# Kernel tuning notes

Measured on AMD Instinct MI355X. Metric: run time of the kernel, lower is better.

The kernel has to match this reference:

```python
import jax, jax.numpy as jnp
import numpy as np

H, D, BETA = 12, 64, 1.0
EPS = 1e-8


def setup_inputs() -> dict:
    key = jax.random.key(0)
    k1, k2 = jax.random.split(key)
    n, dim = 1024, H * D
    x = jax.random.normal(k1, (n, dim), dtype=jnp.float32)
    mask = jnp.ones((n, n), dtype=bool)
    W_qk = jax.random.normal(k2, (2 * H * D, dim), dtype=jnp.float32) / np.sqrt(dim).astype(np.float32)
    return {"x": x, "mask": mask, "W_qk": W_qk}


def _free_energy_heads(xh, mask, W_qk):
    # xh: (H, n, D) unit-norm token vectors per head -> per-head free energy (H,)
    n = xh.shape[1]
    xf = jnp.transpose(xh, (1, 0, 2)).reshape(n, H * D)      # 'h n d -> n (h d)'
    qk = xf @ W_qk.T                                          # (n, 2*H*D), Linear no-bias
    q, k = jnp.split(qk, 2, axis=-1)
    q = jnp.transpose(q.reshape(n, H, D), (1, 0, 2))          # (H, n, D)
    k = jnp.transpose(k.reshape(n, H, D), (1, 0, 2))
    sim = jnp.einsum('hid,hjd->hij', q, k)                    # (H, n, n)
    sim = jnp.where(mask, sim, jnp.finfo(sim.dtype).min)
    J = jax.scipy.special.logsumexp(sim, axis=-1)             # (H, n)
    # t* = root of quadratic: beta*t^2 + (-0.5 - 2 beta J) t + (beta J^2 + 0.5 J - 0.25 beta |x|^2)
    hn = jnp.sum(xh * xh, axis=-1)                            # (H, n), |x_i|^2
    b = -0.5 - 2.0 * BETA * J
    c = BETA * J ** 2 + 0.5 * J - 0.25 * BETA * hn
    t = (-b + jnp.sqrt(b * b - 4.0 * BETA * c)) / (2.0 * BETA)
    v = t - J                                                 # (H, n)
    inv_v = 1.0 / jnp.clip(v, EPS, jnp.finfo(v.dtype).max)    # safe_reciprocal
    phi = (BETA * jnp.sum(t, axis=-1)
           - 0.5 * jnp.sum(jnp.log(v + EPS), axis=-1)
           + 0.25 * BETA * jnp.sum(hn * inv_v, axis=-1))      # (H,)
    log_Z = -0.5 * n * (1.0 + jnp.log(2.0 * BETA)) + phi
    return -log_Z / BETA                                      # (H,)


def reference(x, mask, W_qk):
    n = x.shape[0]
    xh = jnp.transpose(x.reshape(n, H, D), (1, 0, 2))         # (H, n, D)
    xh = xh / jnp.linalg.norm(xh, axis=-1, keepdims=True)
    jac = jax.jacrev(lambda xs: _free_energy_heads(xs, mask, W_qk))(xh)  # (H, H, n, D)
    diag = jnp.diagonal(jac)                                  # (n, D, H): dF_h/dx_h only
    out = jnp.transpose(diag, (0, 2, 1)).reshape(n, H * D)    # 'n d h -> n (h d)'
    return -out
```

## Files before the change

kernel.cpp:

```cpp
#include <hip/hip_runtime.h>
#include <cstdint>

#define NTOK 1024
#define NH   12
#define HD   64
#define DIM  768
#define QKD  1536

static constexpr float C2G = 0.61803398874989485f;

typedef __bf16 bf16x8 __attribute__((ext_vector_type(8)));
typedef __bf16 bf16x4 __attribute__((ext_vector_type(4)));
typedef float  f32x4  __attribute__((ext_vector_type(4)));

#define MFMA16(a, b, c) __builtin_amdgcn_mfma_f32_16x16x32_bf16((a), (b), (c), 0, 0, 0)

#define FRAG(S, outer, ks) (*(const bf16x8*)&S[(outer) + (l & 15)][(ks) * 32 + (l >> 4) * 8])

__global__ __launch_bounds__(256) void prep_k(const float* __restrict__ x,
                                              const float* __restrict__ W,
                                              float* __restrict__ xf,
                                              __bf16* __restrict__ xhb,
                                              __bf16* __restrict__ Wb,
                                              __bf16* __restrict__ WT) {
  __shared__ float Ws[64][65];
  int b = blockIdx.x, t = threadIdx.x;
  if (b < 3072) {
    int gid  = b * 4 + (t >> 6);
    int lane = t & 63;
    int i = gid / NH, h = gid - i * NH;
    size_t idx = (size_t)i * DIM + h * HD + lane;
    float v = x[idx];
    float ss = v * v;
#pragma unroll
    for (int m = 1; m < 64; m <<= 1) ss += __shfl_xor(ss, m);
    float r = v * rsqrtf(ss);
    xf[idx] = r;
    xhb[idx] = (__bf16)r;
  } else if (b < 3072 + 1152) {
    int tg = (b - 3072) * 256 + t;
    float4 v = ((const float4*)W)[tg];
    bf16x4 o;
    o[0] = (__bf16)v.x; o[1] = (__bf16)v.y; o[2] = (__bf16)v.z; o[3] = (__bf16)v.w;
    *(bf16x4*)(Wb + (size_t)tg * 4) = o;
  } else {
    int bb = b - 3072 - 1152;
    int h = bb % NH, p = bb / NH;
    int rowbase = p * DIM + h * HD;
#pragma unroll
    for (int rr = 0; rr < 16; ++rr) {
      int row = rr * 4 + (t >> 6), col = t & 63;
      Ws[row][col] = W[(size_t)(rowbase + row) * DIM + h * HD + col];
    }
    __syncthreads();
    __bf16* dst = WT + ((size_t)p * NH + h) * HD * HD;
#pragma unroll
    for (int rr = 0; rr < 16; ++rr) {
      int dlt = rr * 4 + (t >> 6), d = t & 63;
      dst[dlt * HD + d] = (__bf16)Ws[d][dlt];
    }
  }
}

__global__ __launch_bounds__(256) void gemm_dual_k(const __bf16* __restrict__ A,
                                                   const __bf16* __restrict__ Bt,
                                                   __bf16* __restrict__ qkb,
                                                   __bf16* __restrict__ qkT) {
  __shared__ __align__(16) __bf16 As[64][72];
  __shared__ __align__(16) __bf16 Bs[64][72];
  int m0 = blockIdx.x * 64, n0 = blockIdx.y * 64;
  int t = threadIdx.x, l = t & 63, w = t >> 6;
  int R = (w >> 1) * 32, Cc = (w & 1) * 32;
  int srow = t >> 2, scol = (t & 3) * 16;
  f32x4 acc[2][2] = {};
  for (int k0 = 0; k0 < DIM; k0 += 64) {
    *(uint4*)&As[srow][scol]     = *(const uint4*)(A  + (size_t)(m0 + srow) * DIM + k0 + scol);
    *(uint4*)&As[srow][scol + 8] = *(const uint4*)(A  + (size_t)(m0 + srow) * DIM + k0 + scol + 8);
    *(uint4*)&Bs[srow][scol]     = *(const uint4*)(Bt + (size_t)(n0 + srow) * DIM + k0 + scol);
    *(uint4*)&Bs[srow][scol + 8] = *(const uint4*)(Bt + (size_t)(n0 + srow) * DIM + k0 + scol + 8);
    __syncthreads();
#pragma unroll
    for (int ks = 0; ks < 2; ++ks) {
      bf16x8 af[2], bf[2];
#pragma unroll
      for (int mf = 0; mf < 2; ++mf) af[mf] = FRAG(As, R + mf * 16, ks);
#pragma unroll
      for (int nf = 0; nf < 2; ++nf) bf[nf] = FRAG(Bs, Cc + nf * 16, ks);
#pragma unroll
      for (int mf = 0; mf < 2; ++mf)
#pragma unroll
        for (int nf = 0; nf < 2; ++nf) acc[mf][nf] = MFMA16(af[mf], bf[nf], acc[mf][nf]);
    }
    __syncthreads();
  }
#pragma unroll
  for (int mf = 0; mf < 2; ++mf)
#pragma unroll
    for (int nf = 0; nf < 2; ++nf) {
      int rowb = m0 + R + mf * 16 + (l >> 4) * 4;
      int col  = n0 + Cc + nf * 16 + (l & 15);
      bf16x4 o4;
#pragma unroll
      for (int r = 0; r < 4; ++r) {
        __bf16 v = (__bf16)acc[mf][nf][r];
        o4[r] = v;
        qkb[(size_t)(rowb + r) * QKD + col] = v;
      }
      *(bf16x4*)(qkT + (size_t)col * NTOK + rowb) = o4;
    }
}

__global__ __launch_bounds__(256) void kbar_k(const __bf16* __restrict__ qkb,
                                              const __bf16* __restrict__ qkT,
                                              __bf16* __restrict__ kbar,
                                              float* __restrict__ invZ) {
  __shared__ __align__(16) __bf16 Qs[64][72], Ks[2][64][72], KTs[2][64][72], Es[64][72];
  __shared__ float Zs[64];
  int i0 = blockIdx.x * 64, h = blockIdx.y;
  int t = threadIdx.x, l = t & 63, w = t >> 6;
  int R = (w >> 1) * 32, Cc = (w & 1) * 32;
  int srow = t >> 2, scol = (t & 3) * 16;
  const __bf16* kbase  = qkb + DIM + h * HD;
  const __bf16* ktbase = qkT + (size_t)(DIM + h * HD + srow) * NTOK;
  *(uint4*)&Qs[srow][scol]     = *(const uint4*)(qkb + (size_t)(i0 + srow) * QKD + h * HD + scol);
  *(uint4*)&Qs[srow][scol + 8] = *(const uint4*)(qkb + (size_t)(i0 + srow) * QKD + h * HD + scol + 8);
  if (t < 64) Zs[t] = 0.f;
  uint4 kA = *(const uint4*)(kbase + (size_t)srow * QKD + scol);
  uint4 kB = *(const uint4*)(kbase + (size_t)srow * QKD + scol + 8);
  uint4 tA = *(const uint4*)(ktbase + scol);
  uint4 tB = *(const uint4*)(ktbase + scol + 8);
  f32x4 facc[2][2] = {};
  float zacc[8] = {0.f, 0.f, 0.f, 0.f, 0.f, 0.f, 0.f, 0.f};
  for (int jt = 0; jt < 16; ++jt) {
    int buf = jt & 1;
    *(uint4*)&Ks[buf][srow][scol]      = kA;
    *(uint4*)&Ks[buf][srow][scol + 8]  = kB;
    *(uint4*)&KTs[buf][srow][scol]     = tA;
    *(uint4*)&KTs[buf][srow][scol + 8] = tB;
    if (jt < 15) {
      int j0 = (jt + 1) * 64;
      kA = *(const uint4*)(kbase + (size_t)(j0 + srow) * QKD + scol);
      kB = *(const uint4*)(kbase + (size_t)(j0 + srow) * QKD + scol + 8);
      tA = *(const uint4*)(ktbase + j0 + scol);
      tB = *(const uint4*)(ktbase + j0 + scol + 8);
    }
    __syncthreads();
    f32x4 sacc[2][2] = {};
#pragma unroll
    for (int ks = 0; ks < 2; ++ks) {
      bf16x8 af[2], bf[2];
#pragma unroll
      for (int mf = 0; mf < 2; ++mf) af[mf] = FRAG(Qs, R + mf * 16, ks);
#pragma unroll
      for (int nf = 0; nf < 2; ++nf) bf[nf] = FRAG(Ks[buf], Cc + nf * 16, ks);
#pragma unroll
      for (int mf = 0; mf < 2; ++mf)
#pragma unroll
        for (int nf = 0; nf < 2; ++nf) sacc[mf][nf] = MFMA16(af[mf], bf[nf], sacc[mf][nf]);
    }
#pragma unroll
    for (int mf = 0; mf < 2; ++mf)
#pragma unroll
      for (int r = 0; r < 4; ++r) {
        float e0 = __expf(sacc[mf][0][r]);
        float e1 = __expf(sacc[mf][1][r]);
        zacc[mf * 4 + r] += e0 + e1;
        int row = R + mf * 16 + (l >> 4) * 4 + r;
        Es[row][Cc + (l & 15)]      = (__bf16)e0;
        Es[row][Cc + 16 + (l & 15)] = (__bf16)e1;
      }
    __syncthreads();
#pragma unroll
    for (int ks = 0; ks < 2; ++ks) {
      bf16x8 af[2], bf[2];
#pragma unroll
      for (int mf = 0; mf < 2; ++mf) af[mf] = FRAG(Es, R + mf * 16, ks);
#pragma unroll
      for (int nf = 0; nf < 2; ++nf) bf[nf] = FRAG(KTs[buf], Cc + nf * 16, ks);
#pragma unroll
      for (int mf = 0; mf < 2; ++mf)
#pragma unroll
        for (int nf = 0; nf < 2; ++nf) facc[mf][nf] = MFMA16(af[mf], bf[nf], facc[mf][nf]);
    }
  }
#pragma unroll
  for (int zi = 0; zi < 8; ++zi) {
    float z = zacc[zi];
    z += __shfl_xor(z, 1); z += __shfl_xor(z, 2);
    z += __shfl_xor(z, 4); z += __shfl_xor(z, 8);
    if ((l & 15) == 0) {
      int row = R + (zi >> 2) * 16 + (l >> 4) * 4 + (zi & 3);
      atomicAdd(&Zs[row], z);
    }
  }
  __syncthreads();
  if (t < 64) {
    float iz = 1.0f / Zs[t];
    Zs[t] = iz;
    invZ[(size_t)h * NTOK + i0 + t] = iz;
  }
  __syncthreads();
#pragma unroll
  for (int mf = 0; mf < 2; ++mf)
#pragma unroll
    for (int nf = 0; nf < 2; ++nf)
#pragma unroll
      for (int r = 0; r < 4; ++r) {
        int row = R + mf * 16 + (l >> 4) * 4 + r;
        int col = Cc + nf * 16 + (l & 15);
        kbar[(size_t)(i0 + row) * DIM + h * HD + col] = (__bf16)(facc[mf][nf][r] * Zs[row]);
      }
}

__global__ __launch_bounds__(256) void qbar_final_k(const __bf16* __restrict__ qkb,
                                                    const __bf16* __restrict__ qkT,
                                                    const float* __restrict__ invZ,
                                                    const __bf16* __restrict__ kbar,
                                                    const __bf16* __restrict__ WT,
                                                    const float* __restrict__ xf,
                                                    float* __restrict__ out) {
  __shared__ __align__(16) __bf16 Ks[64][72], Qs[2][64][72], QTs[2][64][72], Es[64][72];
  int j0 = blockIdx.x * 64, h = blockIdx.y;
  int t = threadIdx.x, l = t & 63, w = t >> 6;
  int R = (w >> 1) * 32, Cc = (w & 1) * 32;
  int srow = t >> 2, scol = (t & 3) * 16;
  const __bf16* qbase  = qkb + h * HD;
  const __bf16* qtbase = qkT + (size_t)(h * HD + srow) * NTOK;
  const float*  izb    = invZ + (size_t)h * NTOK;
  *(uint4*)&Ks[srow][scol]     = *(const uint4*)(qkb + (size_t)(j0 + srow) * QKD + DIM + h * HD + scol);
  *(uint4*)&Ks[srow][scol + 8] = *(const uint4*)(qkb + (size_t)(j0 + srow) * QKD + DIM + h * HD + scol + 8);
  uint4 qA = *(const uint4*)(qbase + (size_t)srow * QKD + scol);
  uint4 qB = *(const uint4*)(qbase + (size_t)srow * QKD + scol + 8);
  uint4 tA = *(const uint4*)(qtbase + scol);
  uint4 tB = *(const uint4*)(qtbase + scol + 8);
  f32x4 facc[2][2] = {};
  for (int it = 0; it < 16; ++it) {
    int buf = it & 1;
    *(uint4*)&Qs[buf][srow][scol]      = qA;
    *(uint4*)&Qs[buf][srow][scol + 8]  = qB;
    *(uint4*)&QTs[buf][srow][scol]     = tA;
    *(uint4*)&QTs[buf][srow][scol + 8] = tB;
    if (it < 15) {
      int i0 = (it + 1) * 64;
      qA = *(const uint4*)(qbase + (size_t)(i0 + srow) * QKD + scol);
      qB = *(const uint4*)(qbase + (size_t)(i0 + srow) * QKD + scol + 8);
      tA = *(const uint4*)(qtbase + i0 + scol);
      tB = *(const uint4*)(qtbase + i0 + scol + 8);
    }
    __syncthreads();
    f32x4 sacc[2][2] = {};
#pragma unroll
    for (int ks = 0; ks < 2; ++ks) {
      bf16x8 af[2], bf[2];
#pragma unroll
      for (int mf = 0; mf < 2; ++mf) af[mf] = FRAG(Ks, R + mf * 16, ks);
#pragma unroll
      for (int nf = 0; nf < 2; ++nf) bf[nf] = FRAG(Qs[buf], Cc + nf * 16, ks);
#pragma unroll
      for (int mf = 0; mf < 2; ++mf)
#pragma unroll
        for (int nf = 0; nf < 2; ++nf) sacc[mf][nf] = MFMA16(af[mf], bf[nf], sacc[mf][nf]);
    }
    float iz0 = izb[it * 64 + Cc + (l & 15)];
    float iz1 = izb[it * 64 + Cc + 16 + (l & 15)];
#pragma unroll
    for (int mf = 0; mf < 2; ++mf)
#pragma unroll
      for (int r = 0; r < 4; ++r) {
        float e0 = __expf(sacc[mf][0][r]) * iz0;
        float e1 = __expf(sacc[mf][1][r]) * iz1;
        int row = R + mf * 16 + (l >> 4) * 4 + r;
        Es[row][Cc + (l & 15)]      = (__bf16)e0;
        Es[row][Cc + 16 + (l & 15)] = (__bf16)e1;
      }
    __syncthreads();
#pragma unroll
    for (int ks = 0; ks < 2; ++ks) {
      bf16x8 af[2], bf[2];
#pragma unroll
      for (int mf = 0; mf < 2; ++mf) af[mf] = FRAG(Es, R + mf * 16, ks);
#pragma unroll
      for (int nf = 0; nf < 2; ++nf) bf[nf] = FRAG(QTs[buf], Cc + nf * 16, ks);
#pragma unroll
      for (int mf = 0; mf < 2; ++mf)
#pragma unroll
        for (int nf = 0; nf < 2; ++nf) facc[mf][nf] = MFMA16(af[mf], bf[nf], facc[mf][nf]);
    }
  }
  __syncthreads();
#pragma unroll
  for (int mf = 0; mf < 2; ++mf)
#pragma unroll
    for (int nf = 0; nf < 2; ++nf)
#pragma unroll
      for (int r = 0; r < 4; ++r)
        Es[R + mf * 16 + (l >> 4) * 4 + r][Cc + nf * 16 + (l & 15)] = (__bf16)facc[mf][nf][r];
  const __bf16* wq = WT + (size_t)h * HD * HD;
  const __bf16* wk = WT + ((size_t)NH + h) * HD * HD;
  *(uint4*)&Ks[srow][scol]         = *(const uint4*)(kbar + (size_t)(j0 + srow) * DIM + h * HD + scol);
  *(uint4*)&Ks[srow][scol + 8]     = *(const uint4*)(kbar + (size_t)(j0 + srow) * DIM + h * HD + scol + 8);
  *(uint4*)&QTs[0][srow][scol]     = *(const uint4*)(wq + (size_t)srow * HD + scol);
  *(uint4*)&QTs[0][srow][scol + 8] = *(const uint4*)(wq + (size_t)srow * HD + scol + 8);
  *(uint4*)&Qs[0][srow][scol]      = *(const uint4*)(wk + (size_t)srow * HD + scol);
  *(uint4*)&Qs[0][srow][scol + 8]  = *(const uint4*)(wk + (size_t)srow * HD + scol + 8);
  __syncthreads();
  f32x4 acc2[2][2] = {};
#pragma unroll
  for (int ks = 0; ks < 2; ++ks) {
    bf16x8 af[2], bf[2];
#pragma unroll
    for (int mf = 0; mf < 2; ++mf) af[mf] = FRAG(Ks, R + mf * 16, ks);
#pragma unroll
    for (int nf = 0; nf < 2; ++nf) bf[nf] = FRAG(QTs[0], Cc + nf * 16, ks);
#pragma unroll
    for (int mf = 0; mf < 2; ++mf)
#pragma unroll
      for (int nf = 0; nf < 2; ++nf) acc2[mf][nf] = MFMA16(af[mf], bf[nf], acc2[mf][nf]);
  }
#pragma unroll
  for (int ks = 0; ks < 2; ++ks) {
    bf16x8 af[2], bf[2];
#pragma unroll
    for (int mf = 0; mf < 2; ++mf) af[mf] = FRAG(Es, R + mf * 16, ks);
#pragma unroll
    for (int nf = 0; nf < 2; ++nf) bf[nf] = FRAG(Qs[0], Cc + nf * 16, ks);
#pragma unroll
    for (int mf = 0; mf < 2; ++mf)
#pragma unroll
      for (int nf = 0; nf < 2; ++nf) acc2[mf][nf] = MFMA16(af[mf], bf[nf], acc2[mf][nf]);
  }
#pragma unroll
  for (int mf = 0; mf < 2; ++mf)
#pragma unroll
    for (int nf = 0; nf < 2; ++nf)
#pragma unroll
      for (int r = 0; r < 4; ++r) {
        int row = j0 + R + mf * 16 + (l >> 4) * 4 + r;
        int col = h * HD + Cc + nf * 16 + (l & 15);
        size_t idx = (size_t)row * DIM + col;
        out[idx] = acc2[mf][nf][r] + C2G * xf[idx];
      }
}

extern "C" void kernel_launch(void* const* d_in, const int* in_sizes, int n_in,
                              void* d_out, int out_size, void* d_ws, size_t ws_size,
                              hipStream_t stream) {
  const float* x = (const float*)d_in[0];
  const float* W = (const float*)d_in[2];
  float* out = (float*)d_out;

  float* wsf = (float*)d_ws;
  size_t off = 0;
  float* xf   = wsf + off; off += (size_t)NTOK * DIM;
  float* invZ = wsf + off; off += (size_t)NH * NTOK;
  __bf16* wsb = (__bf16*)(wsf + off);
  size_t boff = 0;
  __bf16* xhb  = wsb + boff; boff += (size_t)NTOK * DIM;
  __bf16* Wb   = wsb + boff; boff += (size_t)QKD * DIM;
  __bf16* WT   = wsb + boff; boff += (size_t)2 * NH * HD * HD;
  __bf16* qkb  = wsb + boff; boff += (size_t)NTOK * QKD;
  __bf16* qkT  = wsb + boff; boff += (size_t)QKD * NTOK;
  __bf16* kbar = wsb + boff; boff += (size_t)NTOK * DIM;

  prep_k<<<dim3(3072 + 1152 + 24), dim3(256), 0, stream>>>(x, W, xf, xhb, Wb, WT);
  gemm_dual_k<<<dim3(16, 24), dim3(256), 0, stream>>>(xhb, Wb, qkb, qkT);
  kbar_k<<<dim3(16, NH), dim3(256), 0, stream>>>(qkb, qkT, kbar, invZ);
  qbar_final_k<<<dim3(16, NH), dim3(256), 0, stream>>>(qkb, qkT, invZ, kbar, WT, xf, out);
}
```

Measured before the change: 55.92 us.

## Split attention reductions across two blocks and add a separate final combine kernel

The kbar and qbar kernels now split the 1024-long reduction into two halves, which doubles the grid from 192 to 384 blocks. Each block writes fp32 partial accumulators, and the row sums Z are accumulated with global atomics into a buffer that prep_k zeroes. A new final kernel adds the partials, normalises, and applies the W projections. The QK GEMM also gains a double-buffered LDS pipeline with register prefetch, which removes one barrier per k-step. The aim is to fill more of the GPU's compute units, at the cost of an extra launch, extra partial-buffer traffic and atomics.

New measurement: 50.53 us. 1.11x faster.

```diff
diff --git a/kernel.cpp b/kernel.cpp
--- a/kernel.cpp
+++ b/kernel.cpp
@@ -22,7 +22,8 @@
                                               float* __restrict__ xf,
                                               __bf16* __restrict__ xhb,
                                               __bf16* __restrict__ Wb,
-                                              __bf16* __restrict__ WT) {
+                                              __bf16* __restrict__ WT,
+                                              float* __restrict__ Zg) {
   __shared__ float Ws[64][65];
   int b = blockIdx.x, t = threadIdx.x;
   if (b < 3072) {
@@ -37,14 +38,14 @@
     float r = v * rsqrtf(ss);
     xf[idx] = r;
     xhb[idx] = (__bf16)r;
-  } else if (b < 3072 + 1152) {
+  } else if (b < 4224) {
     int tg = (b - 3072) * 256 + t;
     float4 v = ((const float4*)W)[tg];
     bf16x4 o;
     o[0] = (__bf16)v.x; o[1] = (__bf16)v.y; o[2] = (__bf16)v.z; o[3] = (__bf16)v.w;
     *(bf16x4*)(Wb + (size_t)tg * 4) = o;
-  } else {
-    int bb = b - 3072 - 1152;
+  } else if (b < 4248) {
+    int bb = b - 4224;
     int h = bb % NH, p = bb / NH;
     int rowbase = p * DIM + h * HD;
 #pragma unroll
@@ -59,6 +60,10 @@
       int dlt = rr * 4 + (t >> 6), d = t & 63;
       dst[dlt * HD + d] = (__bf16)Ws[d][dlt];
     }
+  } else {
+    int zz = b - 4248;
+    float4 z4 = make_float4(0.f, 0.f, 0.f, 0.f);
+    ((float4*)Zg)[zz * 256 + t] = z4;
   }
 }
 
@@ -66,32 +71,42 @@
                                                    const __bf16* __restrict__ Bt,
                                                    __bf16* __restrict__ qkb,
                                                    __bf16* __restrict__ qkT) {
-  __shared__ __align__(16) __bf16 As[64][72];
-  __shared__ __align__(16) __bf16 Bs[64][72];
+  __shared__ __align__(16) __bf16 As[2][64][72], Bs[2][64][72];
   int m0 = blockIdx.x * 64, n0 = blockIdx.y * 64;
   int t = threadIdx.x, l = t & 63, w = t >> 6;
   int R = (w >> 1) * 32, Cc = (w & 1) * 32;
   int srow = t >> 2, scol = (t & 3) * 16;
+  uint4 aA = *(const uint4*)(A  + (size_t)(m0 + srow) * DIM + scol);
+  uint4 aB = *(const uint4*)(A  + (size_t)(m0 + srow) * DIM + scol + 8);
+  uint4 bA = *(const uint4*)(Bt + (size_t)(n0 + srow) * DIM + scol);
+  uint4 bB = *(const uint4*)(Bt + (size_t)(n0 + srow) * DIM + scol + 8);
   f32x4 acc[2][2] = {};
-  for (int k0 = 0; k0 < DIM; k0 += 64) {
-    *(uint4*)&As[srow][scol]     = *(const uint4*)(A  + (size_t)(m0 + srow) * DIM + k0 + scol);
-    *(uint4*)&As[srow][scol + 8] = *(const uint4*)(A  + (size_t)(m0 + srow) * DIM + k0 + scol + 8);
-    *(uint4*)&Bs[srow][scol]     = *(const uint4*)(Bt + (size_t)(n0 + srow) * DIM + k0 + scol);
-    *(uint4*)&Bs[srow][scol + 8] = *(const uint4*)(Bt + (size_t)(n0 + srow) * DIM + k0 + scol + 8);
+  for (int kt = 0; kt < 12; ++kt) {
+    int buf = kt & 1;
+    *(uint4*)&As[buf][srow][scol]     = aA;
+    *(uint4*)&As[buf][srow][scol + 8] = aB;
+    *(uint4*)&Bs[buf][srow][scol]     = bA;
+    *(uint4*)&Bs[buf][srow][scol + 8] = bB;
+    if (kt < 11) {
+      int k0 = (kt + 1) * 64;
+      aA = *(const uint4*)(A  + (size_t)(m0 + srow) * DIM + k0 + scol);
+      aB = *(const uint4*)(A  + (size_t)(m0 + srow) * DIM + k0 + scol + 8);
+      bA = *(const uint4*)(Bt + (size_t)(n0 + srow) * DIM + k0 + scol);
+      bB = *(const uint4*)(Bt + (size_t)(n0 + srow) * DIM + k0 + scol + 8);
+    }
     __syncthreads();
 #pragma unroll
     for (int ks = 0; ks < 2; ++ks) {
       bf16x8 af[2], bf[2];
 #pragma unroll
-      for (int mf = 0; mf < 2; ++mf) af[mf] = FRAG(As, R + mf * 16, ks);
-#pragma unroll
-      for (int nf = 0; nf < 2; ++nf) bf[nf] = FRAG(Bs, Cc + nf * 16, ks);
+      for (int mf = 0; mf < 2; ++mf) af[mf] = FRAG(As[buf], R + mf * 16, ks);
+#pragma unroll
+      for (int nf = 0; nf < 2; ++nf) bf[nf] = FRAG(Bs[buf], Cc + nf * 16, ks);
 #pragma unroll
       for (int mf = 0; mf < 2; ++mf)
 #pragma unroll
         for (int nf = 0; nf < 2; ++nf) acc[mf][nf] = MFMA16(af[mf], bf[nf], acc[mf][nf]);
     }
-    __syncthreads();
   }
 #pragma unroll
   for (int mf = 0; mf < 2; ++mf)
@@ -110,13 +125,15 @@
     }
 }
 
-__global__ __launch_bounds__(256) void kbar_k(const __bf16* __restrict__ qkb,
-                                              const __bf16* __restrict__ qkT,
-                                              __bf16* __restrict__ kbar,
-                                              float* __restrict__ invZ) {
+__global__ __launch_bounds__(256) void kbarp_k(const __bf16* __restrict__ qkb,
+                                               const __bf16* __restrict__ qkT,
+                                               float* __restrict__ part_k,
+                                               float* __restrict__ Zg) {
   __shared__ __align__(16) __bf16 Qs[64][72], Ks[2][64][72], KTs[2][64][72], Es[64][72];
-  __shared__ float Zs[64];
-  int i0 = blockIdx.x * 64, h = blockIdx.y;
+  int u = blockIdx.x;
+  int h = u >> 5, rem = u & 31;
+  int i0 = (rem >> 1) * 64;
+  int jt0 = (rem & 1) * 8;
   int t = threadIdx.x, l = t & 63, w = t >> 6;
   int R = (w >> 1) * 32, Cc = (w & 1) * 32;
   int srow = t >> 2, scol = (t & 3) * 16;
@@ -124,20 +141,19 @@
   const __bf16* ktbase = qkT + (size_t)(DIM + h * HD + srow) * NTOK;
   *(uint4*)&Qs[srow][scol]     = *(const uint4*)(qkb + (size_t)(i0 + srow) * QKD + h * HD + scol);
   *(uint4*)&Qs[srow][scol + 8] = *(const uint4*)(qkb + (size_t)(i0 + srow) * QKD + h * HD + scol + 8);
-  if (t < 64) Zs[t] = 0.f;
-  uint4 kA = *(const uint4*)(kbase + (size_t)srow * QKD + scol);
-  uint4 kB = *(const uint4*)(kbase + (size_t)srow * QKD + scol + 8);
-  uint4 tA = *(const uint4*)(ktbase + scol);
-  uint4 tB = *(const uint4*)(ktbase + scol + 8);
+  uint4 kA = *(const uint4*)(kbase + (size_t)(jt0 * 64 + srow) * QKD + scol);
+  uint4 kB = *(const uint4*)(kbase + (size_t)(jt0 * 64 + srow) * QKD + scol + 8);
+  uint4 tA = *(const uint4*)(ktbase + jt0 * 64 + scol);
+  uint4 tB = *(const uint4*)(ktbase + jt0 * 64 + scol + 8);
   f32x4 facc[2][2] = {};
   float zacc[8] = {0.f, 0.f, 0.f, 0.f, 0.f, 0.f, 0.f, 0.f};
-  for (int jt = 0; jt < 16; ++jt) {
+  for (int jt = jt0; jt < jt0 + 8; ++jt) {
     int buf = jt & 1;
     *(uint4*)&Ks[buf][srow][scol]      = kA;
     *(uint4*)&Ks[buf][srow][scol + 8]  = kB;
     *(uint4*)&KTs[buf][srow][scol]     = tA;
     *(uint4*)&KTs[buf][srow][scol + 8] = tB;
-    if (jt < 15) {
+    if (jt < jt0 + 7) {
       int j0 = (jt + 1) * 64;
       kA = *(const uint4*)(kbase + (size_t)(j0 + srow) * QKD + scol);
       kB = *(const uint4*)(kbase + (size_t)(j0 + srow) * QKD + scol + 8);
@@ -183,6 +199,17 @@
         for (int nf = 0; nf < 2; ++nf) facc[mf][nf] = MFMA16(af[mf], bf[nf], facc[mf][nf]);
     }
   }
+  float* pk = part_k + (size_t)u * 4096;
+#pragma unroll
+  for (int mf = 0; mf < 2; ++mf)
+#pragma unroll
+    for (int nf = 0; nf < 2; ++nf)
+#pragma unroll
+      for (int r = 0; r < 4; ++r) {
+        int row = R + mf * 16 + (l >> 4) * 4 + r;
+        int col = Cc + nf * 16 + (l & 15);
+        pk[row * 64 + col] = facc[mf][nf][r];
+      }
 #pragma unroll
   for (int zi = 0; zi < 8; ++zi) {
     float z = zacc[zi];
@@ -190,57 +217,40 @@
     z += __shfl_xor(z, 4); z += __shfl_xor(z, 8);
     if ((l & 15) == 0) {
       int row = R + (zi >> 2) * 16 + (l >> 4) * 4 + (zi & 3);
-      atomicAdd(&Zs[row], z);
-    }
-  }
-  __syncthreads();
-  if (t < 64) {
-    float iz = 1.0f / Zs[t];
-    Zs[t] = iz;
-    invZ[(size_t)h * NTOK + i0 + t] = iz;
-  }
-  __syncthreads();
-#pragma unroll
-  for (int mf = 0; mf < 2; ++mf)
-#pragma unroll
-    for (int nf = 0; nf < 2; ++nf)
-#pragma unroll
-      for (int r = 0; r < 4; ++r) {
-        int row = R + mf * 16 + (l >> 4) * 4 + r;
-        int col = Cc + nf * 16 + (l & 15);
-        kbar[(size_t)(i0 + row) * DIM + h * HD + col] = (__bf16)(facc[mf][nf][r] * Zs[row]);
-      }
-}
-
-__global__ __launch_bounds__(256) void qbar_final_k(const __bf16* __restrict__ qkb,
-                                                    const __bf16* __restrict__ qkT,
-                                                    const float* __restrict__ invZ,
-                                                    const __bf16* __restrict__ kbar,
-                                                    const __bf16* __restrict__ WT,
-                                                    const float* __restrict__ xf,
-                                                    float* __restrict__ out) {
+      atomicAdd(&Zg[(size_t)h * NTOK + i0 + row], z);
+    }
+  }
+}
+
+__global__ __launch_bounds__(256) void qbarp_k(const __bf16* __restrict__ qkb,
+                                               const __bf16* __restrict__ qkT,
+                                               const float* __restrict__ Zg,
+                                               float* __restrict__ part_q) {
   __shared__ __align__(16) __bf16 Ks[64][72], Qs[2][64][72], QTs[2][64][72], Es[64][72];
-  int j0 = blockIdx.x * 64, h = blockIdx.y;
+  int u = blockIdx.x;
+  int h = u >> 5, rem = u & 31;
+  int j0 = (rem >> 1) * 64;
+  int it0 = (rem & 1) * 8;
   int t = threadIdx.x, l = t & 63, w = t >> 6;
   int R = (w >> 1) * 32, Cc = (w & 1) * 32;
   int srow = t >> 2, scol = (t & 3) * 16;
   const __bf16* qbase  = qkb + h * HD;
   const __bf16* qtbase = qkT + (size_t)(h * HD + srow) * NTOK;
-  const float*  izb    = invZ + (size_t)h * NTOK;
+  const float*  zb     = Zg + (size_t)h * NTOK;
   *(uint4*)&Ks[srow][scol]     = *(const uint4*)(qkb + (size_t)(j0 + srow) * QKD + DIM + h * HD + scol);
   *(uint4*)&Ks[srow][scol + 8] = *(const uint4*)(qkb + (size_t)(j0 + srow) * QKD + DIM + h * HD + scol + 8);
-  uint4 qA = *(const uint4*)(qbase + (size_t)srow * QKD + scol);
-  uint4 qB = *(const uint4*)(qbase + (size_t)srow * QKD + scol + 8);
-  uint4 tA = *(const uint4*)(qtbase + scol);
-  uint4 tB = *(const uint4*)(qtbase + scol + 8);
+  uint4 qA = *(const uint4*)(qbase + (size_t)(it0 * 64 + srow) * QKD + scol);
+  uint4 qB = *(const uint4*)(qbase + (size_t)(it0 * 64 + srow) * QKD + scol + 8);
+  uint4 tA = *(const uint4*)(qtbase + it0 * 64 + scol);
+  uint4 tB = *(const uint4*)(qtbase + it0 * 64 + scol + 8);
   f32x4 facc[2][2] = {};
-  for (int it = 0; it < 16; ++it) {
+  for (int it = it0; it < it0 + 8; ++it) {
     int buf = it & 1;
     *(uint4*)&Qs[buf][srow][scol]      = qA;
     *(uint4*)&Qs[buf][srow][scol + 8]  = qB;
     *(uint4*)&QTs[buf][srow][scol]     = tA;
     *(uint4*)&QTs[buf][srow][scol + 8] = tB;
-    if (it < 15) {
+    if (it < it0 + 7) {
       int i0 = (it + 1) * 64;
       qA = *(const uint4*)(qbase + (size_t)(i0 + srow) * QKD + scol);
       qB = *(const uint4*)(qbase + (size_t)(i0 + srow) * QKD + scol + 8);
@@ -261,8 +271,8 @@
 #pragma unroll
         for (int nf = 0; nf < 2; ++nf) sacc[mf][nf] = MFMA16(af[mf], bf[nf], sacc[mf][nf]);
     }
-    float iz0 = izb[it * 64 + Cc + (l & 15)];
-    float iz1 = izb[it * 64 + Cc + 16 + (l & 15)];
+    float iz0 = 1.0f / zb[it * 64 + Cc + (l & 15)];
+    float iz1 = 1.0f / zb[it * 64 + Cc + 16 + (l & 15)];
 #pragma unroll
     for (int mf = 0; mf < 2; ++mf)
 #pragma unroll
@@ -287,47 +297,78 @@
         for (int nf = 0; nf < 2; ++nf) facc[mf][nf] = MFMA16(af[mf], bf[nf], facc[mf][nf]);
     }
   }
-  __syncthreads();
+  float* pq = part_q + (size_t)u * 4096;
 #pragma unroll
   for (int mf = 0; mf < 2; ++mf)
 #pragma unroll
     for (int nf = 0; nf < 2; ++nf)
 #pragma unroll
-      for (int r = 0; r < 4; ++r)
-        Es[R + mf * 16 + (l >> 4) * 4 + r][Cc + nf * 16 + (l & 15)] = (__bf16)facc[mf][nf][r];
+      for (int r = 0; r < 4; ++r) {
+        int row = R + mf * 16 + (l >> 4) * 4 + r;
+        int col = Cc + nf * 16 + (l & 15);
+        pq[row * 64 + col] = facc[mf][nf][r];
+      }
+}
+
+__global__ __launch_bounds__(256) void final2_k(const float* __restrict__ part_k,
+                                                const float* __restrict__ part_q,
+                                                const float* __restrict__ Zg,
+                                                const __bf16* __restrict__ WT,
+                                                const float* __restrict__ xf,
+                                                float* __restrict__ out) {
+  __shared__ __align__(16) __bf16 Ka[64][72], Qa[64][72], WqS[64][72], WkS[64][72];
+  int u = blockIdx.x;
+  int h = u >> 4, jidx = u & 15, j0 = jidx * 64;
+  int t = threadIdx.x, l = t & 63, w = t >> 6;
+  int R = (w >> 1) * 32, Cc = (w & 1) * 32;
+  int srow = t >> 2, scol = (t & 3) * 16;
+  const float* pk = part_k + ((size_t)(h * 32 + jidx * 2)) * 4096;
+  const float* pq = part_q + ((size_t)(h * 32 + jidx * 2)) * 4096;
+#pragma unroll
+  for (int mf = 0; mf < 2; ++mf)
+#pragma unroll
+    for (int r = 0; r < 4; ++r) {
+      int row = R + mf * 16 + (l >> 4) * 4 + r;
+      float iz = 1.0f / Zg[(size_t)h * NTOK + j0 + row];
+#pragma unroll
+      for (int nf = 0; nf < 2; ++nf) {
+        int col = Cc + nf * 16 + (l & 15);
+        int off = row * 64 + col;
+        Ka[row][col] = (__bf16)((pk[off] + pk[4096 + off]) * iz);
+        Qa[row][col] = (__bf16)(pq[off] + pq[4096 + off]);
+      }
+    }
   const __bf16* wq = WT + (size_t)h * HD * HD;
   const __bf16* wk = WT + ((size_t)NH + h) * HD * HD;
-  *(uint4*)&Ks[srow][scol]         = *(const uint4*)(kbar + (size_t)(j0 + srow) * DIM + h * HD + scol);
-  *(uint4*)&Ks[srow][scol + 8]     = *(const uint4*)(kbar + (size_t)(j0 + srow) * DIM + h * HD + scol + 8);
-  *(uint4*)&QTs[0][srow][scol]     = *(const uint4*)(wq + (size_t)srow * HD + scol);
-  *(uint4*)&QTs[0][srow][scol + 8] = *(const uint4*)(wq + (size_t)srow * HD + scol + 8);
-  *(uint4*)&Qs[0][srow][scol]      = *(const uint4*)(wk + (size_t)srow * HD + scol);
-  *(uint4*)&Qs[0][srow][scol + 8]  = *(const uint4*)(wk + (size_t)srow * HD + scol + 8);
+  *(uint4*)&WqS[srow][scol]     = *(const uint4*)(wq + (size_t)srow * HD + scol);
+  *(uint4*)&WqS[srow][scol + 8] = *(const uint4*)(wq + (size_t)srow * HD + scol + 8);
+  *(uint4*)&WkS[srow][scol]     = *(const uint4*)(wk + (size_t)srow * HD + scol);
+  *(uint4*)&WkS[srow][scol + 8] = *(const uint4*)(wk + (size_t)srow * HD + scol + 8);
   __syncthreads();
-  f32x4 acc2[2][2] = {};
+  f32x4 acc[2][2] = {};
 #pragma unroll
   for (int ks = 0; ks < 2; ++ks) {
     bf16x8 af[2], bf[2];
 #pragma unroll
-    for (int mf = 0; mf < 2; ++mf) af[mf] = FRAG(Ks, R + mf * 16, ks);
-#pragma unroll
-    for (int nf = 0; nf < 2; ++nf) bf[nf] = FRAG(QTs[0], Cc + nf * 16, ks);
+    for (int mf = 0; mf < 2; ++mf) af[mf] = FRAG(Ka, R + mf * 16, ks);
+#pragma unroll
+    for (int nf = 0; nf < 2; ++nf) bf[nf] = FRAG(WqS, Cc + nf * 16, ks);
 #pragma unroll
     for (int mf = 0; mf < 2; ++mf)
 #pragma unroll
-      for (int nf = 0; nf < 2; ++nf) acc2[mf][nf] = MFMA16(af[mf], bf[nf], acc2[mf][nf]);
+      for (int nf = 0; nf < 2; ++nf) acc[mf][nf] = MFMA16(af[mf], bf[nf], acc[mf][nf]);
   }
 #pragma unroll
   for (int ks = 0; ks < 2; ++ks) {
     bf16x8 af[2], bf[2];
 #pragma unroll
-    for (int mf = 0; mf < 2; ++mf) af[mf] = FRAG(Es, R + mf * 16, ks);
-#pragma unroll
-    for (int nf = 0; nf < 2; ++nf) bf[nf] = FRAG(Qs[0], Cc + nf * 16, ks);
+    for (int mf = 0; mf < 2; ++mf) af[mf] = FRAG(Qa, R + mf * 16, ks);
+#pragma unroll
+    for (int nf = 0; nf < 2; ++nf) bf[nf] = FRAG(WkS, Cc + nf * 16, ks);
 #pragma unroll
     for (int mf = 0; mf < 2; ++mf)
 #pragma unroll
-      for (int nf = 0; nf < 2; ++nf) acc2[mf][nf] = MFMA16(af[mf], bf[nf], acc2[mf][nf]);
+      for (int nf = 0; nf < 2; ++nf) acc[mf][nf] = MFMA16(af[mf], bf[nf], acc[mf][nf]);
   }
 #pragma unroll
   for (int mf = 0; mf < 2; ++mf)
@@ -338,7 +379,7 @@
         int row = j0 + R + mf * 16 + (l >> 4) * 4 + r;
         int col = h * HD + Cc + nf * 16 + (l & 15);
         size_t idx = (size_t)row * DIM + col;
-        out[idx] = acc2[mf][nf][r] + C2G * xf[idx];
+        out[idx] = acc[mf][nf][r] + C2G * xf[idx];
       }
 }
 
@@ -351,19 +392,21 @@
 
   float* wsf = (float*)d_ws;
   size_t off = 0;
-  float* xf   = wsf + off; off += (size_t)NTOK * DIM;
-  float* invZ = wsf + off; off += (size_t)NH * NTOK;
+  float* xf     = wsf + off; off += (size_t)NTOK * DIM;
+  float* Zg     = wsf + off; off += (size_t)NH * NTOK;
+  float* part_k = wsf + off; off += (size_t)384 * 4096;
+  float* part_q = wsf + off; off += (size_t)384 * 4096;
   __bf16* wsb = (__bf16*)(wsf + off);
   size_t boff = 0;
-  __bf16* xhb  = wsb + boff; boff += (size_t)NTOK * DIM;
-  __bf16* Wb   = wsb + boff; boff += (size_t)QKD * DIM;
-  __bf16* WT   = wsb + boff; boff += (size_t)2 * NH * HD * HD;
-  __bf16* qkb  = wsb + boff; boff += (size_t)NTOK * QKD;
-  __bf16* qkT  = wsb + boff; boff += (size_t)QKD * NTOK;
-  __bf16* kbar = wsb + boff; boff += (size_t)NTOK * DIM;
-
-  prep_k<<<dim3(3072 + 1152 + 24), dim3(256), 0, stream>>>(x, W, xf, xhb, Wb, WT);
+  __bf16* xhb = wsb + boff; boff += (size_t)NTOK * DIM;
+  __bf16* Wb  = wsb + boff; boff += (size_t)QKD * DIM;
+  __bf16* WT  = wsb + boff; boff += (size_t)2 * NH * HD * HD;
+  __bf16* qkb = wsb + boff; boff += (size_t)NTOK * QKD;
+  __bf16* qkT = wsb + boff; boff += (size_t)QKD * NTOK;
+
+  prep_k<<<dim3(4260), dim3(256), 0, stream>>>(x, W, xf, xhb, Wb, WT, Zg);
   gemm_dual_k<<<dim3(16, 24), dim3(256), 0, stream>>>(xhb, Wb, qkb, qkT);
-  kbar_k<<<dim3(16, NH), dim3(256), 0, stream>>>(qkb, qkT, kbar, invZ);
-  qbar_final_k<<<dim3(16, NH), dim3(256), 0, stream>>>(qkb, qkT, invZ, kbar, WT, xf, out);
-}
+  kbarp_k<<<dim3(384), dim3(256), 0, stream>>>(qkb, qkT, part_k, Zg);
+  qbarp_k<<<dim3(384), dim3(256), 0, stream>>>(qkb, qkT, Zg, part_q);
+  final2_k<<<dim3(192), dim3(256), 0, stream>>>(part_k, part_q, Zg, WT, xf, out);
+}
```
